# Optimization experiments

Measured on AMD Instinct MI355X. Metric: run time of the kernel, lower is better.

The kernel has to match this reference:

```python
import jax, jax.numpy as jnp
import numpy as np

H = 8          # heads
KP = 6         # num_sparse keypoint tokens per group
NUM_PATCHES = 256


def _build_mask(N, Nk):
    # mask_q: [H, 3, N] bool, query token (g=0, i=0) disabled
    mask_q = np.ones((H, 3, N), dtype=bool)
    mask_q[:, 0, 0] = False
    # mask_k: [H, 3, Nk] bool, key token j=0 disabled for all groups
    mask_k = np.ones((H, 3, Nk), dtype=bool)
    mask_k[:, :, 0] = False
    keep = mask_q[:, :, :, None] & mask_k[:, :, None, :]  # [H,3,N,Nk]
    return jnp.asarray(~keep)  # True where masked out


def setup_inputs() -> dict:
    key = jax.random.key(0)
    k1, k2, k3 = jax.random.split(key, 3)
    B, G, N, D = 64, 3, NUM_PATCHES + KP, 512
    x = jax.random.normal(k1, (B, G, N, D), dtype=jnp.float32)
    w_qkv = jax.random.normal(k2, (D, 3 * D), dtype=jnp.float32) * (D ** -0.5)
    w_out = jax.random.normal(k3, (D, D), dtype=jnp.float32) * (D ** -0.5)
    b_out = jnp.zeros((D,), dtype=jnp.float32)
    return {"x": x, "w_qkv": w_qkv, "w_out": w_out, "b_out": b_out}


def reference(x, w_qkv, w_out, b_out):
    B, G, N, D = x.shape
    Dh = D // H
    scale = D ** -0.5  # scale_with_head=False

    qkv = x @ w_qkv  # [B,G,N,3D]
    q, k, v = jnp.split(qkv, 3, axis=-1)

    def to_heads(t):  # b g n (h d) -> b h g n d
        return t.reshape(B, G, N, H, Dh).transpose(0, 3, 1, 2, 4)

    q, k, v = to_heads(q), to_heads(k), to_heads(v)

    # gather keypoint K/V from all groups, shared across every group
    k_kp = k[:, :, :, :KP].reshape(B, H, 1, G * KP, Dh)
    v_kp = v[:, :, :, :KP].reshape(B, H, 1, G * KP, Dh)
    k_kp = jnp.broadcast_to(k_kp, (B, H, G, G * KP, Dh))
    v_kp = jnp.broadcast_to(v_kp, (B, H, G, G * KP, Dh))
    k = jnp.concatenate([k_kp, k[:, :, :, KP:]], axis=3)  # [B,H,G,Nk,Dh]
    v = jnp.concatenate([v_kp, v[:, :, :, KP:]], axis=3)
    Nk = k.shape[3]

    dots = jnp.einsum('bhgid,bhgjd->bhgij', q, k) * scale
    masked = _build_mask(N, Nk)  # [H,3,N,Nk], broadcasts over B
    neg = -jnp.finfo(dots.dtype).max
    dots = jnp.where(masked[None], neg, dots)

    attn = jax.nn.softmax(dots, axis=-1)
    out = jnp.einsum('bhgij,bhgjd->bhgid', attn, v)
    out = out.transpose(0, 2, 3, 1, 4).reshape(B, G, N, D)  # b h g n d -> b g n (h d)
    out = out @ w_out + b_out
    return out, dots
```

## Files before the change

### kernel.cpp

```cpp
#include <hip/hip_runtime.h>
#include <float.h>
#include <math.h>

#define B_   64
#define G_   3
#define N_   262
#define D_   512
#define H_   8
#define DH   64
#define KP_  6
#define NKP  18
#define NK   274
#define TD3  1536
#define M_   50304
#define SCALE 0.044194173824159216f
#define LOG2E 1.4426950408889634f

typedef unsigned short u16;
typedef __attribute__((ext_vector_type(4))) float f32x4;
typedef __attribute__((ext_vector_type(2))) float f32x2;
typedef float f32x4u __attribute__((ext_vector_type(4), aligned(4)));
typedef __attribute__((ext_vector_type(8))) short bf16x8;

__device__ __forceinline__ u16 f2bf(float f) {
    unsigned int u = __float_as_uint(f);
    u += 0x7FFFu + ((u >> 16) & 1u);
    return (u16)(u >> 16);
}
__device__ __forceinline__ unsigned pack2bf(float lo, float hi) {
    unsigned ul = __float_as_uint(lo); ul += 0x7FFFu + ((ul >> 16) & 1u);
    unsigned uh = __float_as_uint(hi); uh += 0x7FFFu + ((uh >> 16) & 1u);
    return (ul >> 16) | (uh & 0xFFFF0000u);
}
__device__ __forceinline__ float mask_val() { return __uint_as_float(0xFF7F0000u); }

__device__ __forceinline__ void gload16(const void* g, void* l) {
    __builtin_amdgcn_global_load_lds(
        (const __attribute__((address_space(1))) unsigned int*)g,
        (__attribute__((address_space(3))) unsigned int*)l, 16, 0, 0);
}

__device__ __forceinline__ int xcd_swz(int orig, int nwg) {
    int q = nwg >> 3, r = nwg & 7;
    int xcd = orig & 7, lin = orig >> 3;
    return (xcd < r ? xcd * (q + 1) : r * (q + 1) + (xcd - r) * q) + lin;
}

__global__ __launch_bounds__(256)
void tcast(const float* __restrict__ w, u16* __restrict__ wT, int K, int N)
{
    int idx = blockIdx.x * 256 + threadIdx.x;
    if (idx < K * N) {
        int nn = idx / K, kk = idx - nn * K;
        wT[idx] = f2bf(w[(size_t)kk * N + nn]);
    }
}

template<int AF32, int OUT_BF16>
__global__ __launch_bounds__(512)
void gemm_bf16(const float* __restrict__ Af, const u16* __restrict__ Ab,
               const u16* __restrict__ WT,
               float* __restrict__ Cf, u16* __restrict__ Cb,
               const float* __restrict__ bias, int Ndim, int Kdim)
{
    __shared__ u16 Asm[128 * 64];
    __shared__ u16 Bsm[256 * 64];

    const int tid  = threadIdx.x;
    const int lane = tid & 63;
    const int wid  = tid >> 6;
    const int l15  = lane & 15;
    const int lg   = lane >> 4;
    const int wr   = (wid & 1) * 64;
    const int wc   = (wid >> 1) * 64;

    const int GX   = Ndim / 256;
    const int v    = xcd_swz(blockIdx.x, gridDim.x);
    const int row0 = (v / GX) * 128;
    const int col0 = (v % GX) * 256;

    const float* fsrcA[2];
    const u16*   bsrcA[2];
    #pragma unroll
    for (int i = 0; i < 2; ++i) {
        int slot = i * 512 + tid;
        int r = slot >> 3;
        int sblk = (slot & 7) ^ (r & 7);
        if (AF32) fsrcA[i] = Af + (size_t)(row0 + r) * Kdim + sblk * 8;
        else      bsrcA[i] = Ab + (size_t)(row0 + r) * Kdim + sblk * 8;
    }
    const u16* srcB[4];
    #pragma unroll
    for (int i = 0; i < 4; ++i) {
        int slot = i * 512 + tid;
        int r = slot >> 3;
        int sblk = (slot & 7) ^ (r & 7);
        srcB[i] = WT + (size_t)(col0 + r) * Kdim + sblk * 8;
    }

    f32x4 acc[4][4] = {};

    for (int k0 = 0; k0 < Kdim; k0 += 64) {
        #pragma unroll
        for (int i = 0; i < 4; ++i)
            gload16(srcB[i] + k0, &Bsm[(i * 512 + wid * 64) * 8]);
        if (AF32) {
            #pragma unroll
            for (int i = 0; i < 2; ++i) {
                float4 v0 = *(const float4*)(fsrcA[i] + k0);
                float4 v1 = *(const float4*)(fsrcA[i] + k0 + 4);
                u16 t[8] = { f2bf(v0.x), f2bf(v0.y), f2bf(v0.z), f2bf(v0.w),
                             f2bf(v1.x), f2bf(v1.y), f2bf(v1.z), f2bf(v1.w) };
                *(uint4*)&Asm[(i * 512 + tid) * 8] = *(const uint4*)t;
            }
        } else {
            #pragma unroll
            for (int i = 0; i < 2; ++i)
                gload16(bsrcA[i] + k0, &Asm[(i * 512 + wid * 64) * 8]);
        }
        __syncthreads();
        #pragma unroll
        for (int kk = 0; kk < 2; ++kk) {
            const int xb = (kk * 4 + lg) ^ (l15 & 7);
            bf16x8 a[4], b[4];
            #pragma unroll
            for (int m = 0; m < 4; ++m) a[m] = *(const bf16x8*)&Asm[(wr + m * 16 + l15) * 64 + xb * 8];
            #pragma unroll
            for (int n = 0; n < 4; ++n) b[n] = *(const bf16x8*)&Bsm[(wc + n * 16 + l15) * 64 + xb * 8];
            #pragma unroll
            for (int m = 0; m < 4; ++m)
                #pragma unroll
                for (int n = 0; n < 4; ++n)
                    acc[m][n] = __builtin_amdgcn_mfma_f32_16x16x32_bf16(a[m], b[n], acc[m][n], 0, 0, 0);
        }
        __syncthreads();
    }

    const int rbase = row0 + wr + lg * 4;
    const int cbase = col0 + wc + l15;
    #pragma unroll
    for (int m = 0; m < 4; ++m)
        #pragma unroll
        for (int n = 0; n < 4; ++n) {
            const int col = cbase + n * 16;
            #pragma unroll
            for (int r = 0; r < 4; ++r) {
                const int row = rbase + m * 16 + r;
                float vv = acc[m][n][r];
                if (OUT_BF16) Cb[(size_t)row * Ndim + col] = f2bf(vv);
                else          Cf[(size_t)row * Ndim + col] = vv + bias[col];
            }
        }
}

__global__ __launch_bounds__(768, 1)
void attn_bf16(const u16* __restrict__ qkv, float* __restrict__ dots,
               u16* __restrict__ otmp)
{
    __shared__ u16 Ks[288 * 72];
    __shared__ u16 Vt[64 * 296];
    __shared__ float rowbuf[12][4 * 276];

    const int tid  = threadIdx.x;
    const int lane = tid & 63;
    const int wid  = tid >> 6;
    const int l15  = lane & 15;
    const int lg   = lane >> 4;

    const int bhg = blockIdx.x;
    const int b   = bhg / (H_ * G_);
    const int h   = (bhg / G_) % H_;
    const int g   = bhg % G_;
    const int rowbase = (b * G_ + g) * N_;
    const size_t dbase0 = (((size_t)(b * H_ + h) * G_ + g) * N_) * NK;

    #pragma unroll
    for (int it = 0; it < 3; ++it) {
        int lin = tid + it * 768;
        {
            int tok = lin >> 3, kg = (lin & 7) << 3;
            uint4 kv = make_uint4(0, 0, 0, 0), vv = make_uint4(0, 0, 0, 0);
            if (tok < NK) {
                int gs, ns;
                if (tok < NKP) { gs = tok / KP_; ns = tok - gs * KP_; }
                else           { gs = g;         ns = tok - NKP + KP_; }
                const u16* p = qkv + ((size_t)((b * G_ + gs) * N_ + ns)) * TD3 + h * DH + kg;
                kv = *(const uint4*)(p + D_);
                vv = *(const uint4*)(p + 2 * D_);
            }
            *(uint4*)&Ks[tok * 72 + kg] = kv;
            int slot = ((tok >> 5) << 5) | (((tok & 15) >> 2) << 3) | (((tok >> 4) & 1) << 2) | (tok & 3);
            union { uint4 u4; u16 us[8]; } u; u.u4 = vv;
            #pragma unroll
            for (int e = 0; e < 8; ++e) Vt[(kg + e) * 296 + slot] = u.us[e];
        }
    }
    __syncthreads();

    float* rb = rowbuf[wid];

    for (int t = wid; t < 17; t += 12) {
        const int n0 = t * 16;
        int qrow = n0 + l15; if (qrow > N_ - 1) qrow = N_ - 1;
        const u16* qp = qkv + (size_t)(rowbase + qrow) * TD3 + h * DH;
        bf16x8 qa0 = *(const bf16x8*)(qp + lg * 8);
        bf16x8 qa1 = *(const bf16x8*)(qp + 32 + lg * 8);

        f32x4 c[18];
        __builtin_amdgcn_s_setprio(1);
        #pragma unroll
        for (int jt = 0; jt < 18; ++jt) {
            const u16* kr = &Ks[(jt * 16 + l15) * 72];
            bf16x8 kb0 = *(const bf16x8*)(kr + lg * 8);
            bf16x8 kb1 = *(const bf16x8*)(kr + 32 + lg * 8);
            f32x4 z = {};
            z = __builtin_amdgcn_mfma_f32_16x16x32_bf16(kb0, qa0, z, 0, 0, 0);
            c[jt] = __builtin_amdgcn_mfma_f32_16x16x32_bf16(kb1, qa1, z, 0, 0, 0);
        }
        __builtin_amdgcn_s_setprio(0);

        #pragma unroll
        for (int jt = 0; jt < 18; ++jt)
            #pragma unroll
            for (int rr = 0; rr < 4; ++rr) c[jt][rr] *= SCALE;
        c[0][0] = (lg == 0) ? mask_val() : c[0][0];
        if (g == 0 && t == 0) {
            #pragma unroll
            for (int jt = 0; jt < 18; ++jt)
                #pragma unroll
                for (int rr = 0; rr < 4; ++rr)
                    c[jt][rr] = (l15 == 0) ? mask_val() : c[jt][rr];
        }

        const int php = l15 >> 2;
        const int r4  = l15 & 3;
        #pragma unroll
        for (int ph = 0; ph < 4; ++ph) {
            if (php == ph) {
                float* rr_ = &rb[r4 * 276];
                #pragma unroll
                for (int jt = 0; jt < 17; ++jt)
                    *(f32x4*)&rr_[jt * 16 + 4 * lg] = c[jt];
                if (lg == 0) { f32x2 tl = { c[17][0], c[17][1] }; *(f32x2*)&rr_[272] = tl; }
            }
            const int base_row = n0 + 4 * ph;
            #pragma unroll
            for (int r = 0; r < 4; ++r) {
                const int row = base_row + r;
                if (row < N_) {
                    const float* rrb = &rb[r * 276];
                    float* gp = &dots[dbase0 + (size_t)row * NK];
                    #pragma unroll
                    for (int i2 = 0; i2 < 2; ++i2) {
                        int ch = lane + (i2 << 6);
                        if (ch < 68) {
                            f32x4u vv = *(const f32x4*)&rrb[ch * 4];
                            __builtin_nontemporal_store(vv, (f32x4u*)&gp[ch * 4]);
                        } else if (ch == 68) {
                            f32x2 v2 = *(const f32x2*)&rrb[272];
                            __builtin_nontemporal_store(v2, (f32x2*)&gp[272]);
                        }
                    }
                }
            }
        }

        c[17][2] = -INFINITY; c[17][3] = -INFINITY;
        c[17][0] = (lg == 0) ? c[17][0] : -INFINITY;
        c[17][1] = (lg == 0) ? c[17][1] : -INFINITY;

        float mx = c[0][0];
        #pragma unroll
        for (int jt = 0; jt < 18; ++jt)
            #pragma unroll
            for (int rr = 0; rr < 4; ++rr) mx = fmaxf(mx, c[jt][rr]);
        mx = fmaxf(mx, __shfl_xor(mx, 16, 64));
        mx = fmaxf(mx, __shfl_xor(mx, 32, 64));
        float s = 0.f;
        #pragma unroll
        for (int jt = 0; jt < 18; ++jt)
            #pragma unroll
            for (int rr = 0; rr < 4; ++rr) {
                float p = exp2f((c[jt][rr] - mx) * LOG2E);
                c[jt][rr] = p;
                s += p;
            }
        s += __shfl_xor(s, 16, 64);
        s += __shfl_xor(s, 32, 64);
        const float inv = 1.f / s;

        f32x4 o[4] = {};
        __builtin_amdgcn_s_setprio(1);
        #pragma unroll
        for (int sl = 0; sl < 9; ++sl) {
            union { bf16x8 v; unsigned u[4]; } pa;
            pa.u[0] = pack2bf(c[2 * sl][0],     c[2 * sl][1]);
            pa.u[1] = pack2bf(c[2 * sl][2],     c[2 * sl][3]);
            pa.u[2] = pack2bf(c[2 * sl + 1][0], c[2 * sl + 1][1]);
            pa.u[3] = pack2bf(c[2 * sl + 1][2], c[2 * sl + 1][3]);
            #pragma unroll
            for (int dt = 0; dt < 4; ++dt) {
                bf16x8 vb = *(const bf16x8*)&Vt[(dt * 16 + l15) * 296 + sl * 32 + lg * 8];
                o[dt] = __builtin_amdgcn_mfma_f32_16x16x32_bf16(pa.v, vb, o[dt], 0, 0, 0);
            }
        }
        __builtin_amdgcn_s_setprio(0);

        u16* ob = (u16*)rb;
        #pragma unroll
        for (int dt = 0; dt < 4; ++dt)
            #pragma unroll
            for (int rr = 0; rr < 4; ++rr) {
                const int q = lg * 4 + rr;
                const float iq = __shfl(inv, q, 64);
                ob[q * 64 + dt * 16 + l15] = f2bf(o[dt][rr] * iq);
            }
        {
            const int vrows = min(16, N_ - n0);
            const int nch = vrows * 8;
            #pragma unroll
            for (int i2 = 0; i2 < 2; ++i2) {
                int ch = lane + (i2 << 6);
                if (ch < nch) {
                    int r = ch >> 3, cp = ch & 7;
                    uint4 vv = *(const uint4*)&ob[ch * 8];
                    *(uint4*)(otmp + (size_t)(rowbase + n0 + r) * D_ + h * DH + cp * 8) = vv;
                }
            }
        }
    }
}

extern "C" void kernel_launch(void* const* d_in, const int* in_sizes, int n_in,
                              void* d_out, int out_size, void* d_ws, size_t ws_size,
                              hipStream_t stream)
{
    const float* x     = (const float*)d_in[0];
    const float* w_qkv = (const float*)d_in[1];
    const float* w_out = (const float*)d_in[2];
    const float* b_out = (const float*)d_in[3];

    float* out  = (float*)d_out;
    float* dots = out + (size_t)M_ * D_;

    u16* wqkvT = (u16*)d_ws;
    u16* woutT = wqkvT + (size_t)TD3 * D_;
    u16* qkvb  = woutT + (size_t)D_ * D_;
    u16* otmpb = qkvb  + (size_t)M_ * TD3;

    tcast<<<(TD3 * D_ + 255) / 256, 256, 0, stream>>>(w_qkv, wqkvT, D_, TD3);
    tcast<<<(D_ * D_ + 255) / 256, 256, 0, stream>>>(w_out, woutT, D_, D_);

    gemm_bf16<1, 1><<<(TD3 / 256) * (M_ / 128), 512, 0, stream>>>(
        x, nullptr, wqkvT, nullptr, qkvb, nullptr, TD3, D_);

    attn_bf16<<<dim3(B_ * H_ * G_), 768, 0, stream>>>(qkvb, dots, otmpb);

    gemm_bf16<0, 0><<<(D_ / 256) * (M_ / 128), 512, 0, stream>>>(
        nullptr, otmpb, woutT, out, nullptr, b_out, D_, D_);
}
```

Before: 343.0 us.

## Stage bf16 GEMM output through LDS for vectorized nontemporal stores, fuse weight casts

The QKV GEMM epilogue now packs its bf16 accumulators into shared memory and writes each row chunk with 16-byte nontemporal stores, replacing scattered 2-byte stores. The attention kernel's output stores also become nontemporal. The two weight transpose-cast kernels are merged into one launch. The aim is to cut store transaction count and launch overhead, at the cost of extra LDS traffic and possibly losing L2 residency for qkv data the attention kernel reads next.

```diff
diff --git a/kernel.cpp b/kernel.cpp
--- a/kernel.cpp
+++ b/kernel.cpp
@@ -20,6 +20,7 @@
 typedef __attribute__((ext_vector_type(4))) float f32x4;
 typedef __attribute__((ext_vector_type(2))) float f32x2;
 typedef float f32x4u __attribute__((ext_vector_type(4), aligned(4)));
+typedef __attribute__((ext_vector_type(4))) unsigned int u32x4;
 typedef __attribute__((ext_vector_type(8))) short bf16x8;
 
 __device__ __forceinline__ u16 f2bf(float f) {
@@ -47,12 +48,19 @@
 }
 
 __global__ __launch_bounds__(256)
-void tcast(const float* __restrict__ w, u16* __restrict__ wT, int K, int N)
+void tcast2(const float* __restrict__ w1, u16* __restrict__ wT1,
+            const float* __restrict__ w2, u16* __restrict__ wT2)
 {
     int idx = blockIdx.x * 256 + threadIdx.x;
-    if (idx < K * N) {
-        int nn = idx / K, kk = idx - nn * K;
-        wT[idx] = f2bf(w[(size_t)kk * N + nn]);
+    if (idx < TD3 * D_) {
+        int nn = idx / D_, kk = idx - nn * D_;
+        wT1[idx] = f2bf(w1[(size_t)kk * TD3 + nn]);
+    } else {
+        int j = idx - TD3 * D_;
+        if (j < D_ * D_) {
+            int nn = j / D_, kk = j - nn * D_;
+            wT2[j] = f2bf(w2[(size_t)kk * D_ + nn]);
+        }
     }
 }
 
@@ -136,6 +144,31 @@
         __syncthreads();
     }
 
+    if (OUT_BF16) {
+        u16* ob = (wid < 4) ? &Asm[wid * 2048] : &Bsm[(wid - 4) * 2048];
+        #pragma unroll
+        for (int p = 0; p < 2; ++p) {
+            #pragma unroll
+            for (int mh = 0; mh < 2; ++mh) {
+                const int m = 2 * p + mh;
+                #pragma unroll
+                for (int n = 0; n < 4; ++n)
+                    #pragma unroll
+                    for (int r = 0; r < 4; ++r)
+                        ob[(mh * 16 + lg * 4 + r) * 64 + n * 16 + l15] = f2bf(acc[m][n][r]);
+            }
+            #pragma unroll
+            for (int it = 0; it < 4; ++it) {
+                const int ch = it * 64 + lane;
+                const int rw = ch >> 3, cp = ch & 7;
+                u32x4 vv = *(const u32x4*)&ob[rw * 64 + cp * 8];
+                __builtin_nontemporal_store(vv,
+                    (u32x4*)(Cb + (size_t)(row0 + wr + p * 32 + rw) * Ndim + col0 + wc + cp * 8));
+            }
+        }
+        return;
+    }
+
     const int rbase = row0 + wr + lg * 4;
     const int cbase = col0 + wc + l15;
     #pragma unroll
@@ -146,9 +179,7 @@
             #pragma unroll
             for (int r = 0; r < 4; ++r) {
                 const int row = rbase + m * 16 + r;
-                float vv = acc[m][n][r];
-                if (OUT_BF16) Cb[(size_t)row * Ndim + col] = f2bf(vv);
-                else          Cf[(size_t)row * Ndim + col] = vv + bias[col];
+                Cf[(size_t)row * Ndim + col] = acc[m][n][r] + bias[col];
             }
         }
 }
@@ -323,8 +354,9 @@
                 int ch = lane + (i2 << 6);
                 if (ch < nch) {
                     int r = ch >> 3, cp = ch & 7;
-                    uint4 vv = *(const uint4*)&ob[ch * 8];
-                    *(uint4*)(otmp + (size_t)(rowbase + n0 + r) * D_ + h * DH + cp * 8) = vv;
+                    u32x4 vv = *(const u32x4*)&ob[ch * 8];
+                    __builtin_nontemporal_store(vv,
+                        (u32x4*)(otmp + (size_t)(rowbase + n0 + r) * D_ + h * DH + cp * 8));
                 }
             }
         }
@@ -348,8 +380,8 @@
     u16* qkvb  = woutT + (size_t)D_ * D_;
     u16* otmpb = qkvb  + (size_t)M_ * TD3;
 
-    tcast<<<(TD3 * D_ + 255) / 256, 256, 0, stream>>>(w_qkv, wqkvT, D_, TD3);
-    tcast<<<(D_ * D_ + 255) / 256, 256, 0, stream>>>(w_out, woutT, D_, D_);
+    tcast2<<<(TD3 * D_ + D_ * D_ + 255) / 256, 256, 0, stream>>>(
+        w_qkv, wqkvT, w_out, woutT);
 
     gemm_bf16<1, 1><<<(TD3 / 256) * (M_ / 128), 512, 0, stream>>>(
         x, nullptr, wqkvT, nullptr, qkvb, nullptr, TD3, D_);
```

Measured after the change: 352.8 us. +2.9%, slower.
